# Performance work log

Measured on AMD Instinct MI355X. Metric: run time of the kernel, lower is better.

The kernel has to match this reference:

```python
import jax, jax.numpy as jnp
import numpy as np
from jax import lax


def extract_patches(x, kh, kw, sh, sw):
    # x: [B,H,W,C] -> [B,oh,ow,kh,kw,C], same element order as tf.image.extract_patches
    B, H, W, C = x.shape
    oh = (H - kh) // sh + 1
    ow = (W - kw) // sw + 1
    rows = jnp.arange(oh)[:, None] * sh + jnp.arange(kh)[None, :]  # [oh,kh]
    cols = jnp.arange(ow)[:, None] * sw + jnp.arange(kw)[None, :]  # [ow,kw]
    p = x[:, rows]            # [B,oh,kh,W,C]
    p = p[:, :, :, cols]      # [B,oh,kh,ow,kw,C]
    return jnp.transpose(p, (0, 1, 3, 2, 4, 5))  # [B,oh,ow,kh,kw,C]


def fastgrnn(x, W, U, bg, bu, zeta, nu):
    # FastGRNN: z=sigmoid(Wx+Uh+bg); c=tanh(Wx+Uh+bu); h'=z*h+(sig(zeta)*(1-z)+sig(nu))*c
    # x: [N,T,D] -> final hidden [N,H]
    wx = jnp.einsum('ntd,dh->nth', x, W)  # precompute input projection
    z_gate = jax.nn.sigmoid(zeta)
    n_gate = jax.nn.sigmoid(nu)

    def step(h, wx_t):
        pre = wx_t + h @ U
        z = jax.nn.sigmoid(pre + bg)
        c = jnp.tanh(pre + bu)
        h_new = z * h + (z_gate * (1.0 - z) + n_gate) * c
        return h_new, None

    h0 = jnp.zeros((x.shape[0], W.shape[1]), x.dtype)
    hT, _ = lax.scan(step, h0, jnp.swapaxes(wx, 0, 1))  # scan over T
    return hT


def rnnpool_forward(inputs, W1, U1, bg1, bu1, zeta1, nu1,
                    W2, U2, bg2, bu2, zeta2, nu2, kh, kw, sh, sw):
    B, H, Wd, C = inputs.shape
    oh = (H - kh) // sh + 1
    ow = (Wd - kw) // sw + 1
    patches = extract_patches(inputs, kh, kw, sh, sw)          # [B,oh,ow,kh,kw,C]
    N = B * oh * ow
    p = patches.reshape(N, kh, kw, C)

    u = W1.shape[1]
    # row-wise: rnn1 scans along cols within each row
    x = p.reshape(N * kh, kw, C)
    h = fastgrnn(x, W1, U1, bg1, bu1, zeta1, nu1).reshape(N, kh, u)
    o21 = fastgrnn(h, W2, U2, bg2, bu2, zeta2, nu2)
    o22 = fastgrnn(h[:, ::-1, :], W2, U2, bg2, bu2, zeta2, nu2)

    # col-wise: transpose patch, rnn1 scans along rows within each col
    xc = jnp.transpose(p, (0, 2, 1, 3)).reshape(N * kw, kh, C)
    hc = fastgrnn(xc, W1, U1, bg1, bu1, zeta1, nu1).reshape(N, kw, u)
    o23 = fastgrnn(hc, W2, U2, bg2, bu2, zeta2, nu2)
    o24 = fastgrnn(hc[:, ::-1, :], W2, U2, bg2, bu2, zeta2, nu2)

    out = jnp.concatenate([o21, o22, o23, o24], axis=1)        # [N, 4*hOut]
    return out.reshape(B, oh, ow, -1)


def setup_inputs() -> dict:
    key = jax.random.key(0)
    ks = jax.random.split(key, 9)
    C, u, hout = 16, 8, 16  # in-channels, rnn1 hidden, rnn2 hidden (out_channel//4)
    s = 0.1
    inp = {
        'inputs': jax.random.normal(ks[0], (32, 112, 112, C), jnp.float32),
        'W1': jax.random.normal(ks[1], (C, u), jnp.float32) * s,
        'U1': jax.random.normal(ks[2], (u, u), jnp.float32) * s,
        'bg1': jnp.ones((u,), jnp.float32),
        'bu1': jnp.ones((u,), jnp.float32),
        'zeta1': jnp.float32(100.0),
        'nu1': jnp.float32(-100.0),
        'W2': jax.random.normal(ks[3], (u, hout), jnp.float32) * s,
        'U2': jax.random.normal(ks[4], (hout, hout), jnp.float32) * s,
        'bg2': jnp.ones((hout,), jnp.float32),
        'bu2': jnp.ones((hout,), jnp.float32),
        'zeta2': jnp.float32(100.0),
        'nu2': jnp.float32(-100.0),
        'kh': 8, 'kw': 8, 'sh': 4, 'sw': 4,
    }
    return inp


def reference(inputs, W1, U1, bg1, bu1, zeta1, nu1,
              W2, U2, bg2, bu2, zeta2, nu2, kh, kw, sh, sw):
    return rnnpool_forward(inputs, W1, U1, bg1, bu1, zeta1, nu1,
                           W2, U2, bg2, bu2, zeta2, nu2, kh, kw, sh, sw)
```

## Files before the change

kernel.cpp:

```cpp
#include <hip/hip_runtime.h>

#define PPB 4

typedef float v2f __attribute__((ext_vector_type(2)));

__device__ __forceinline__ float frcp(float x) { return __builtin_amdgcn_rcpf(x); }

__device__ __forceinline__ v2f vfma2(v2f a, v2f b, v2f c) {
#if __has_builtin(__builtin_elementwise_fma)
  return __builtin_elementwise_fma(a, b, c);
#else
  v2f d; d.x = fmaf(a.x, b.x, c.x); d.y = fmaf(a.y, b.y, c.y); return d;
#endif
}
__device__ __forceinline__ v2f vmul2(v2f a, v2f b) { return a * b; }
__device__ __forceinline__ v2f vadd2(v2f a, v2f b) { return a + b; }
__device__ __forceinline__ v2f bc(float x) { v2f p; p.x = x; p.y = x; return p; }

__device__ __forceinline__ v2f gate2(v2f pre, v2f h, v2f bgB, v2f KB, v2f nzgB,
                                     v2f AB, bool first) {
  v2f a = vadd2(pre, bgB);
  v2f s; s.x = __expf(-a.x); s.y = __expf(-a.y);
  v2f one = bc(1.f);
  v2f zd = vadd2(s, one);
  v2f z; z.x = frcp(zd.x); z.y = frcp(zd.y);
  v2f u = vmul2(vmul2(s, s), KB);
  v2f cd = vadd2(u, one);
  v2f cr; cr.x = frcp(cd.x); cr.y = frcp(cd.y);
  v2f cc = vfma2(cr, bc(2.f), bc(-1.f));
  v2f m = vfma2(z, nzgB, AB);
  v2f mc = vmul2(m, cc);
  return first ? mc : vfma2(z, h, mc);
}

__global__ __launch_bounds__(256, 4) void l1_kernel(
    const float* __restrict__ inp, const float* __restrict__ W1,
    const float* __restrict__ U1, const float* __restrict__ bg1,
    const float* __restrict__ bu1, const float* __restrict__ zeta1,
    const float* __restrict__ nu1, float* __restrict__ hrowg,
    float* __restrict__ hcolg) {
  constexpr int ST = 98;

  __shared__ float w1s[128];
  __shared__ float wxs[112 * ST];

  const int tid = threadIdx.x;
  const int bid = blockIdx.x;
  const bool isrow = bid < 448;
  const int v = isrow ? bid : bid - 448;
  const int b = v / 14, wp = v % 14;
  const int base4 = 8 * wp;
  const int span = (wp == 13) ? 8 : 12;

  if (tid < 32) ((float4*)w1s)[tid] = ((const float4*)W1)[tid];
  __syncthreads();

  for (int p = tid; p < 1344; p += 256) {
    int q, s;
    if (isrow) { q = p / 12;  s = p % 12; }
    else       { q = p % 112; s = p / 112; }
    if (s < span) {
      const float* px = isrow
          ? inp + ((size_t)(b * 112 + q) * 112 + base4 + s) * 16
          : inp + ((size_t)(b * 112 + base4 + s) * 112 + q) * 16;
      float4 x0 = ((const float4*)px)[0], x1 = ((const float4*)px)[1],
             x2 = ((const float4*)px)[2], x3 = ((const float4*)px)[3];
      float xr[16] = {x0.x, x0.y, x0.z, x0.w, x1.x, x1.y, x1.z, x1.w,
                      x2.x, x2.y, x2.z, x2.w, x3.x, x3.y, x3.z, x3.w};
      float a0 = 0.f, a1 = 0.f, a2 = 0.f, a3 = 0.f,
            a4 = 0.f, a5 = 0.f, a6 = 0.f, a7 = 0.f;
#pragma unroll
      for (int ci = 0; ci < 16; ++ci) {
        float4 wL = *(const float4*)&w1s[ci * 8];
        float4 wH = *(const float4*)&w1s[ci * 8 + 4];
        a0 = fmaf(xr[ci], wL.x, a0); a1 = fmaf(xr[ci], wL.y, a1);
        a2 = fmaf(xr[ci], wL.z, a2); a3 = fmaf(xr[ci], wL.w, a3);
        a4 = fmaf(xr[ci], wH.x, a4); a5 = fmaf(xr[ci], wH.y, a5);
        a6 = fmaf(xr[ci], wH.z, a6); a7 = fmaf(xr[ci], wH.w, a7);
      }
      float* wd = &wxs[q * ST + s * 8];
      ((float2*)wd)[0] = float2{a0, a1};
      ((float2*)wd)[1] = float2{a2, a3};
      ((float2*)wd)[2] = float2{a4, a5};
      ((float2*)wd)[3] = float2{a6, a7};
    }
  }

  float u1r[8][8];
#pragma unroll
  for (int i = 0; i < 8; i += 2) {
    float4 r0 = ((const float4*)U1)[i * 2 + 0];
    float4 r1 = ((const float4*)U1)[i * 2 + 1];
    float4 r2 = ((const float4*)U1)[i * 2 + 2];
    float4 r3 = ((const float4*)U1)[i * 2 + 3];
    u1r[i][0] = r0.x; u1r[i][1] = r0.y; u1r[i][2] = r0.z; u1r[i][3] = r0.w;
    u1r[i][4] = r1.x; u1r[i][5] = r1.y; u1r[i][6] = r1.z; u1r[i][7] = r1.w;
    u1r[i+1][0] = r2.x; u1r[i+1][1] = r2.y; u1r[i+1][2] = r2.z; u1r[i+1][3] = r2.w;
    u1r[i+1][4] = r3.x; u1r[i+1][5] = r3.y; u1r[i+1][6] = r3.z; u1r[i+1][7] = r3.w;
  }
  float bgv[8], Kc[8];
#pragma unroll
  for (int j = 0; j < 8; ++j) {
    bgv[j] = bg1[j];
    Kc[j] = __expf(2.f * (bg1[j] - bu1[j]));
  }
  const float zg = frcp(1.f + __expf(-zeta1[0]));
  const float ng = frcp(1.f + __expf(-nu1[0]));
  const float A = zg + ng;

  __syncthreads();

  const int nact = (wp == 13) ? 112 : 224;
  if (tid < nact) {
    const int wl = tid / 112, r = tid % 112;
    const int base = r * ST + wl * 32;
    float h[8];
    {
      const float* w0p = &wxs[base];
#pragma unroll
      for (int j = 0; j < 8; ++j) {
        float s = __expf(-(w0p[j] + bgv[j]));
        float z = frcp(1.f + s);
        float u = s * s * Kc[j];
        float c = fmaf(2.f, frcp(1.f + u), -1.f);
        float m = fmaf(-zg, z, A);
        h[j] = m * c;
      }
    }
#pragma unroll
    for (int t = 1; t < 8; ++t) {
      const float* wtp = &wxs[base + t * 8];
      float qa[8];
#pragma unroll
      for (int j = 0; j < 8; ++j) {
        float q = u1r[0][j] * h[0];
        q = fmaf(u1r[1][j], h[1], q);
        q = fmaf(u1r[2][j], h[2], q);
        q = fmaf(u1r[3][j], h[3], q);
        q = fmaf(u1r[4][j], h[4], q);
        q = fmaf(u1r[5][j], h[5], q);
        q = fmaf(u1r[6][j], h[6], q);
        q = fmaf(u1r[7][j], h[7], q);
        qa[j] = q;
      }
#pragma unroll
      for (int j = 0; j < 8; ++j) {
        float pre = wtp[j] + qa[j];
        float s = __expf(-(pre + bgv[j]));
        float z = frcp(1.f + s);
        float u = s * s * Kc[j];
        float c = fmaf(2.f, frcp(1.f + u), -1.f);
        float m = fmaf(-zg, z, A);
        h[j] = fmaf(z, h[j], m * c);
      }
    }
    float* dst = (isrow ? hrowg : hcolg) +
                 ((size_t)(b * 27 + 2 * wp + wl) * 112 + r) * 8;
    ((float4*)dst)[0] = float4{h[0], h[1], h[2], h[3]};
    ((float4*)dst)[1] = float4{h[4], h[5], h[6], h[7]};
  }
}

__global__ __launch_bounds__(256) void l2_kernel(
    const float* __restrict__ hrowg, const float* __restrict__ hcolg,
    const float* __restrict__ W2, const float* __restrict__ U2,
    const float* __restrict__ bg2, const float* __restrict__ bu2,
    const float* __restrict__ zeta2, const float* __restrict__ nu2,
    float* __restrict__ out) {
  constexpr int GST = 18;
  constexpr int WHT = 18;
  __shared__ v2f hbI[PPB][128];
  __shared__ v2f whb[PPB][2 * 8 * WHT];
  __shared__ v2f h2I[PPB][3 * GST + 16];

  const int tid = threadIdx.x, wv = tid >> 6, lane = tid & 63;
  const int w = blockIdx.x * PPB + wv;
  const int n0 = 2 * w, n1 = n0 + 1;

  {
    const int p = lane >> 5, half = (lane >> 4) & 1, idx = lane & 15;
    const int pn = p ? n1 : n0;
    const int pw = pn % 27;
    const int qq = pn / 27;
    const int ph = qq % 27, bb = qq / 27;
    const float* src = half ? &hcolg[(((size_t)(bb * 27 + ph)) * 112 + pw * 4) * 8]
                            : &hrowg[(((size_t)(bb * 27 + pw)) * 112 + ph * 4) * 8];
    float4 val = ((const float4*)src)[idx];
    float* base = (float*)&hbI[wv][half * 64 + idx * 4];
    base[0 + p] = val.x;
    base[2 + p] = val.y;
    base[4 + p] = val.z;
    base[6 + p] = val.w;
  }
  __builtin_amdgcn_wave_barrier();

  const int g = lane >> 4, j = lane & 15;
  v2f w2b[8], u2b[16];
#pragma unroll
  for (int d = 0; d < 8; ++d) w2b[d] = bc(W2[d * 16 + j]);
#pragma unroll
  for (int i = 0; i < 16; ++i) u2b[i] = bc(U2[i * 16 + j]);
  const float bg2v = bg2[j], bu2v = bu2[j];
  const float zg2 = frcp(1.f + __expf(-zeta2[0]));
  const float ng2 = frcp(1.f + __expf(-nu2[0]));
  const v2f bgB = bc(bg2v);
  const v2f KB = bc(__expf(2.f * (bg2v - bu2v)));
  const v2f nzgB = bc(-zg2);
  const v2f AB = bc(zg2 + ng2);

  const int src = g >> 1;

  {
    const v2f* hb = &hbI[wv][src * 64];
    const int t0 = (g & 1) * 4;
#pragma unroll
    for (int i = 0; i < 4; ++i) {
      const int t = t0 + i;
      const v2f* hr = &hb[t * 8];
      v2f p = vmul2(hr[0], w2b[0]);
#pragma unroll
      for (int d = 1; d < 8; ++d) p = vfma2(hr[d], w2b[d], p);
      whb[wv][(src * 8 + t) * WHT + j] = p;
    }
  }
  __builtin_amdgcn_wave_barrier();

  const v2f* whsrc = &whb[wv][src * 8 * WHT];
  v2f* h2q = &h2I[wv][g * GST];

  v2f h2 = bc(0.f);
  {
    const int tt = (g & 1) ? 7 : 0;
    v2f p = whsrc[tt * WHT + j];
    h2 = gate2(p, h2, bgB, KB, nzgB, AB, true);
    h2q[j] = h2;
  }
  __builtin_amdgcn_wave_barrier();
#pragma unroll
  for (int t = 1; t < 8; ++t) {
    const int tt = (g & 1) ? (7 - t) : t;
    v2f p = whsrc[tt * WHT + j];
    const float4* q4 = (const float4*)h2q;
    float4 v0 = q4[0], v1 = q4[1], v2_ = q4[2], v3 = q4[3];
    float4 v4 = q4[4], v5 = q4[5], v6 = q4[6], v7 = q4[7];
    v2f q = vmul2(v2f{v0.x, v0.y}, u2b[0]);
    q = vfma2(v2f{v0.z, v0.w}, u2b[1], q);
    q = vfma2(v2f{v1.x, v1.y}, u2b[2], q);
    q = vfma2(v2f{v1.z, v1.w}, u2b[3], q);
    q = vfma2(v2f{v2_.x, v2_.y}, u2b[4], q);
    q = vfma2(v2f{v2_.z, v2_.w}, u2b[5], q);
    q = vfma2(v2f{v3.x, v3.y}, u2b[6], q);
    q = vfma2(v2f{v3.z, v3.w}, u2b[7], q);
    q = vfma2(v2f{v4.x, v4.y}, u2b[8], q);
    q = vfma2(v2f{v4.z, v4.w}, u2b[9], q);
    q = vfma2(v2f{v5.x, v5.y}, u2b[10], q);
    q = vfma2(v2f{v5.z, v5.w}, u2b[11], q);
    q = vfma2(v2f{v6.x, v6.y}, u2b[12], q);
    q = vfma2(v2f{v6.z, v6.w}, u2b[13], q);
    q = vfma2(v2f{v7.x, v7.y}, u2b[14], q);
    q = vfma2(v2f{v7.z, v7.w}, u2b[15], q);
    v2f pre = vadd2(p, q);
    h2 = gate2(pre, h2, bgB, KB, nzgB, AB, false);
    if (t < 7) {
      h2q[j] = h2;
      __builtin_amdgcn_wave_barrier();
    }
  }

  out[(size_t)n0 * 64 + lane] = h2.x;
  out[(size_t)n1 * 64 + lane] = h2.y;
}

extern "C" void kernel_launch(void* const* d_in, const int* in_sizes, int n_in,
                              void* d_out, int out_size, void* d_ws, size_t ws_size,
                              hipStream_t stream) {
  const float* inp   = (const float*)d_in[0];
  const float* W1    = (const float*)d_in[1];
  const float* U1    = (const float*)d_in[2];
  const float* bg1   = (const float*)d_in[3];
  const float* bu1   = (const float*)d_in[4];
  const float* zeta1 = (const float*)d_in[5];
  const float* nu1   = (const float*)d_in[6];
  const float* W2    = (const float*)d_in[7];
  const float* U2    = (const float*)d_in[8];
  const float* bg2   = (const float*)d_in[9];
  const float* bu2   = (const float*)d_in[10];
  const float* zeta2 = (const float*)d_in[11];
  const float* nu2   = (const float*)d_in[12];
  float* out = (float*)d_out;

  const size_t HSZ = (size_t)32 * 27 * 112 * 8;
  float* hrowg = (float*)d_ws;
  float* hcolg = hrowg + HSZ;

  l1_kernel<<<dim3(896), dim3(256), 0, stream>>>(
      inp, W1, U1, bg1, bu1, zeta1, nu1, hrowg, hcolg);
  l2_kernel<<<dim3(2916), dim3(256), 0, stream>>>(
      hrowg, hcolg, W2, U2, bg2, bu2, zeta2, nu2, out);
}
```

Before: 43.51 us.

## Restructure both RNN kernels: per-thread L2 recurrence and batched L1 projection

The layer-2 kernel switches from a lane-per-hidden-unit layout that communicates through LDS with wave barriers to a layout where each thread carries a full 16-wide hidden state in registers for one patch/direction. It reads weights from uniform global memory and prefetches the next timestep's input. The layer-1 input projection now batches six pixels per thread, reads W1 directly from global instead of LDS, and uses stride 97 in shared memory. These changes are meant to remove LDS round-trips and barriers, at the cost of more registers per thread, 16x more FMAs per thread in the recurrence, and fewer threads overall.

New measurement: 58.52 us. 1.34x slower.

```diff
diff --git a/kernel.cpp b/kernel.cpp
--- a/kernel.cpp
+++ b/kernel.cpp
@@ -1,47 +1,14 @@
 #include <hip/hip_runtime.h>
 
-#define PPB 4
-
-typedef float v2f __attribute__((ext_vector_type(2)));
-
 __device__ __forceinline__ float frcp(float x) { return __builtin_amdgcn_rcpf(x); }
 
-__device__ __forceinline__ v2f vfma2(v2f a, v2f b, v2f c) {
-#if __has_builtin(__builtin_elementwise_fma)
-  return __builtin_elementwise_fma(a, b, c);
-#else
-  v2f d; d.x = fmaf(a.x, b.x, c.x); d.y = fmaf(a.y, b.y, c.y); return d;
-#endif
-}
-__device__ __forceinline__ v2f vmul2(v2f a, v2f b) { return a * b; }
-__device__ __forceinline__ v2f vadd2(v2f a, v2f b) { return a + b; }
-__device__ __forceinline__ v2f bc(float x) { v2f p; p.x = x; p.y = x; return p; }
-
-__device__ __forceinline__ v2f gate2(v2f pre, v2f h, v2f bgB, v2f KB, v2f nzgB,
-                                     v2f AB, bool first) {
-  v2f a = vadd2(pre, bgB);
-  v2f s; s.x = __expf(-a.x); s.y = __expf(-a.y);
-  v2f one = bc(1.f);
-  v2f zd = vadd2(s, one);
-  v2f z; z.x = frcp(zd.x); z.y = frcp(zd.y);
-  v2f u = vmul2(vmul2(s, s), KB);
-  v2f cd = vadd2(u, one);
-  v2f cr; cr.x = frcp(cd.x); cr.y = frcp(cd.y);
-  v2f cc = vfma2(cr, bc(2.f), bc(-1.f));
-  v2f m = vfma2(z, nzgB, AB);
-  v2f mc = vmul2(m, cc);
-  return first ? mc : vfma2(z, h, mc);
-}
-
-__global__ __launch_bounds__(256, 4) void l1_kernel(
+__global__ __launch_bounds__(256) void l1_kernel(
     const float* __restrict__ inp, const float* __restrict__ W1,
     const float* __restrict__ U1, const float* __restrict__ bg1,
     const float* __restrict__ bu1, const float* __restrict__ zeta1,
     const float* __restrict__ nu1, float* __restrict__ hrowg,
     float* __restrict__ hcolg) {
-  constexpr int ST = 98;
-
-  __shared__ float w1s[128];
+  constexpr int ST = 97;
   __shared__ float wxs[112 * ST];
 
   const int tid = threadIdx.x;
@@ -52,52 +19,59 @@
   const int base4 = 8 * wp;
   const int span = (wp == 13) ? 8 : 12;
 
-  if (tid < 32) ((float4*)w1s)[tid] = ((const float4*)W1)[tid];
-  __syncthreads();
-
-  for (int p = tid; p < 1344; p += 256) {
+  int qk[6], sk[6];
+  const float* pk[6];
+  bool actk[6];
+#pragma unroll
+  for (int k = 0; k < 6; ++k) {
+    const int p = tid + 256 * k;
     int q, s;
-    if (isrow) { q = p / 12;  s = p % 12; }
+    if (isrow) { q = p / 12;  s = p - 12 * q; }
     else       { q = p % 112; s = p / 112; }
-    if (s < span) {
-      const float* px = isrow
-          ? inp + ((size_t)(b * 112 + q) * 112 + base4 + s) * 16
-          : inp + ((size_t)(b * 112 + base4 + s) * 112 + q) * 16;
-      float4 x0 = ((const float4*)px)[0], x1 = ((const float4*)px)[1],
-             x2 = ((const float4*)px)[2], x3 = ((const float4*)px)[3];
-      float xr[16] = {x0.x, x0.y, x0.z, x0.w, x1.x, x1.y, x1.z, x1.w,
-                      x2.x, x2.y, x2.z, x2.w, x3.x, x3.y, x3.z, x3.w};
-      float a0 = 0.f, a1 = 0.f, a2 = 0.f, a3 = 0.f,
-            a4 = 0.f, a5 = 0.f, a6 = 0.f, a7 = 0.f;
-#pragma unroll
-      for (int ci = 0; ci < 16; ++ci) {
-        float4 wL = *(const float4*)&w1s[ci * 8];
-        float4 wH = *(const float4*)&w1s[ci * 8 + 4];
-        a0 = fmaf(xr[ci], wL.x, a0); a1 = fmaf(xr[ci], wL.y, a1);
-        a2 = fmaf(xr[ci], wL.z, a2); a3 = fmaf(xr[ci], wL.w, a3);
-        a4 = fmaf(xr[ci], wH.x, a4); a5 = fmaf(xr[ci], wH.y, a5);
-        a6 = fmaf(xr[ci], wH.z, a6); a7 = fmaf(xr[ci], wH.w, a7);
-      }
-      float* wd = &wxs[q * ST + s * 8];
-      ((float2*)wd)[0] = float2{a0, a1};
-      ((float2*)wd)[1] = float2{a2, a3};
-      ((float2*)wd)[2] = float2{a4, a5};
-      ((float2*)wd)[3] = float2{a6, a7};
-    }
-  }
+    qk[k] = q; sk[k] = s;
+    actk[k] = (p < 1344) && (s < span);
+    pk[k] = isrow
+        ? inp + ((size_t)(b * 112 + q) * 112 + base4 + s) * 16
+        : inp + ((size_t)(b * 112 + base4 + s) * 112 + q) * 16;
+  }
+
+  float acc[6][8];
+#pragma unroll
+  for (int k = 0; k < 6; ++k)
+#pragma unroll
+    for (int j = 0; j < 8; ++j) acc[k][j] = 0.f;
+
+#pragma unroll 1
+  for (int half = 0; half < 2; ++half) {
+    const float* w1h = W1 + half * 64;
+#pragma unroll
+    for (int k = 0; k < 6; ++k) {
+      if (actk[k]) {
+        const float4* xp = (const float4*)(pk[k] + half * 8);
+        float4 x0 = xp[0], x1 = xp[1];
+        float xr[8] = {x0.x, x0.y, x0.z, x0.w, x1.x, x1.y, x1.z, x1.w};
+#pragma unroll
+        for (int ci = 0; ci < 8; ++ci)
+#pragma unroll
+          for (int j = 0; j < 8; ++j)
+            acc[k][j] = fmaf(xr[ci], w1h[ci * 8 + j], acc[k][j]);
+      }
+    }
+  }
+
+#pragma unroll
+  for (int k = 0; k < 6; ++k)
+    if (actk[k]) {
+      float* wd = &wxs[qk[k] * ST + sk[k] * 8];
+#pragma unroll
+      for (int j = 0; j < 8; ++j) wd[j] = acc[k][j];
+    }
 
   float u1r[8][8];
 #pragma unroll
-  for (int i = 0; i < 8; i += 2) {
-    float4 r0 = ((const float4*)U1)[i * 2 + 0];
-    float4 r1 = ((const float4*)U1)[i * 2 + 1];
-    float4 r2 = ((const float4*)U1)[i * 2 + 2];
-    float4 r3 = ((const float4*)U1)[i * 2 + 3];
-    u1r[i][0] = r0.x; u1r[i][1] = r0.y; u1r[i][2] = r0.z; u1r[i][3] = r0.w;
-    u1r[i][4] = r1.x; u1r[i][5] = r1.y; u1r[i][6] = r1.z; u1r[i][7] = r1.w;
-    u1r[i+1][0] = r2.x; u1r[i+1][1] = r2.y; u1r[i+1][2] = r2.z; u1r[i+1][3] = r2.w;
-    u1r[i+1][4] = r3.x; u1r[i+1][5] = r3.y; u1r[i+1][6] = r3.z; u1r[i+1][7] = r3.w;
-  }
+  for (int i = 0; i < 8; ++i)
+#pragma unroll
+    for (int j = 0; j < 8; ++j) u1r[i][j] = U1[i * 8 + j];
   float bgv[8], Kc[8];
 #pragma unroll
   for (int j = 0; j < 8; ++j) {
@@ -112,14 +86,13 @@
 
   const int nact = (wp == 13) ? 112 : 224;
   if (tid < nact) {
-    const int wl = tid / 112, r = tid % 112;
+    const int wl = tid / 112, r = tid - 112 * wl;
     const int base = r * ST + wl * 32;
     float h[8];
     {
-      const float* w0p = &wxs[base];
 #pragma unroll
       for (int j = 0; j < 8; ++j) {
-        float s = __expf(-(w0p[j] + bgv[j]));
+        float s = __expf(-(wxs[base + j] + bgv[j]));
         float z = frcp(1.f + s);
         float u = s * s * Kc[j];
         float c = fmaf(2.f, frcp(1.f + u), -1.f);
@@ -129,7 +102,6 @@
     }
 #pragma unroll
     for (int t = 1; t < 8; ++t) {
-      const float* wtp = &wxs[base + t * 8];
       float qa[8];
 #pragma unroll
       for (int j = 0; j < 8; ++j) {
@@ -145,7 +117,7 @@
       }
 #pragma unroll
       for (int j = 0; j < 8; ++j) {
-        float pre = wtp[j] + qa[j];
+        float pre = wxs[base + t * 8 + j] + qa[j];
         float s = __expf(-(pre + bgv[j]));
         float z = frcp(1.f + s);
         float u = s * s * Kc[j];
@@ -161,114 +133,91 @@
   }
 }
 
-__global__ __launch_bounds__(256) void l2_kernel(
+__global__ __launch_bounds__(64) void l2_kernel(
     const float* __restrict__ hrowg, const float* __restrict__ hcolg,
     const float* __restrict__ W2, const float* __restrict__ U2,
     const float* __restrict__ bg2, const float* __restrict__ bu2,
     const float* __restrict__ zeta2, const float* __restrict__ nu2,
     float* __restrict__ out) {
-  constexpr int GST = 18;
-  constexpr int WHT = 18;
-  __shared__ v2f hbI[PPB][128];
-  __shared__ v2f whb[PPB][2 * 8 * WHT];
-  __shared__ v2f h2I[PPB][3 * GST + 16];
-
-  const int tid = threadIdx.x, wv = tid >> 6, lane = tid & 63;
-  const int w = blockIdx.x * PPB + wv;
-  const int n0 = 2 * w, n1 = n0 + 1;
-
+  const int lane = threadIdx.x;
+  const int p = lane >> 2, g = lane & 3;
+  const int n = blockIdx.x * 16 + p;
+  const int pw = n % 27;
+  const int q = n / 27;
+  const int ph = q % 27, b = q / 27;
+  const int rev = g & 1;
+
+  const float* hs = (g < 2)
+      ? &hrowg[((size_t)(b * 27 + pw) * 112 + ph * 4) * 8]
+      : &hcolg[((size_t)(b * 27 + ph) * 112 + pw * 4) * 8];
+
+  float bgv[16], Kc[16];
+#pragma unroll
+  for (int j = 0; j < 16; ++j) {
+    bgv[j] = bg2[j];
+    Kc[j] = __expf(2.f * (bg2[j] - bu2[j]));
+  }
+  const float zg = frcp(1.f + __expf(-zeta2[0]));
+  const float ng = frcp(1.f + __expf(-nu2[0]));
+  const float A = zg + ng;
+
+  float h2[16];
+#pragma unroll
+  for (int j = 0; j < 16; ++j) h2[j] = 0.f;
+
+  float cur[8], nxt[8];
   {
-    const int p = lane >> 5, half = (lane >> 4) & 1, idx = lane & 15;
-    const int pn = p ? n1 : n0;
-    const int pw = pn % 27;
-    const int qq = pn / 27;
-    const int ph = qq % 27, bb = qq / 27;
-    const float* src = half ? &hcolg[(((size_t)(bb * 27 + ph)) * 112 + pw * 4) * 8]
-                            : &hrowg[(((size_t)(bb * 27 + pw)) * 112 + ph * 4) * 8];
-    float4 val = ((const float4*)src)[idx];
-    float* base = (float*)&hbI[wv][half * 64 + idx * 4];
-    base[0 + p] = val.x;
-    base[2 + p] = val.y;
-    base[4 + p] = val.z;
-    base[6 + p] = val.w;
-  }
-  __builtin_amdgcn_wave_barrier();
-
-  const int g = lane >> 4, j = lane & 15;
-  v2f w2b[8], u2b[16];
-#pragma unroll
-  for (int d = 0; d < 8; ++d) w2b[d] = bc(W2[d * 16 + j]);
-#pragma unroll
-  for (int i = 0; i < 16; ++i) u2b[i] = bc(U2[i * 16 + j]);
-  const float bg2v = bg2[j], bu2v = bu2[j];
-  const float zg2 = frcp(1.f + __expf(-zeta2[0]));
-  const float ng2 = frcp(1.f + __expf(-nu2[0]));
-  const v2f bgB = bc(bg2v);
-  const v2f KB = bc(__expf(2.f * (bg2v - bu2v)));
-  const v2f nzgB = bc(-zg2);
-  const v2f AB = bc(zg2 + ng2);
-
-  const int src = g >> 1;
-
-  {
-    const v2f* hb = &hbI[wv][src * 64];
-    const int t0 = (g & 1) * 4;
-#pragma unroll
-    for (int i = 0; i < 4; ++i) {
-      const int t = t0 + i;
-      const v2f* hr = &hb[t * 8];
-      v2f p = vmul2(hr[0], w2b[0]);
-#pragma unroll
-      for (int d = 1; d < 8; ++d) p = vfma2(hr[d], w2b[d], p);
-      whb[wv][(src * 8 + t) * WHT + j] = p;
-    }
-  }
-  __builtin_amdgcn_wave_barrier();
-
-  const v2f* whsrc = &whb[wv][src * 8 * WHT];
-  v2f* h2q = &h2I[wv][g * GST];
-
-  v2f h2 = bc(0.f);
-  {
-    const int tt = (g & 1) ? 7 : 0;
-    v2f p = whsrc[tt * WHT + j];
-    h2 = gate2(p, h2, bgB, KB, nzgB, AB, true);
-    h2q[j] = h2;
-  }
-  __builtin_amdgcn_wave_barrier();
-#pragma unroll
-  for (int t = 1; t < 8; ++t) {
-    const int tt = (g & 1) ? (7 - t) : t;
-    v2f p = whsrc[tt * WHT + j];
-    const float4* q4 = (const float4*)h2q;
-    float4 v0 = q4[0], v1 = q4[1], v2_ = q4[2], v3 = q4[3];
-    float4 v4 = q4[4], v5 = q4[5], v6 = q4[6], v7 = q4[7];
-    v2f q = vmul2(v2f{v0.x, v0.y}, u2b[0]);
-    q = vfma2(v2f{v0.z, v0.w}, u2b[1], q);
-    q = vfma2(v2f{v1.x, v1.y}, u2b[2], q);
-    q = vfma2(v2f{v1.z, v1.w}, u2b[3], q);
-    q = vfma2(v2f{v2_.x, v2_.y}, u2b[4], q);
-    q = vfma2(v2f{v2_.z, v2_.w}, u2b[5], q);
-    q = vfma2(v2f{v3.x, v3.y}, u2b[6], q);
-    q = vfma2(v2f{v3.z, v3.w}, u2b[7], q);
-    q = vfma2(v2f{v4.x, v4.y}, u2b[8], q);
-    q = vfma2(v2f{v4.z, v4.w}, u2b[9], q);
-    q = vfma2(v2f{v5.x, v5.y}, u2b[10], q);
-    q = vfma2(v2f{v5.z, v5.w}, u2b[11], q);
-    q = vfma2(v2f{v6.x, v6.y}, u2b[12], q);
-    q = vfma2(v2f{v6.z, v6.w}, u2b[13], q);
-    q = vfma2(v2f{v7.x, v7.y}, u2b[14], q);
-    q = vfma2(v2f{v7.z, v7.w}, u2b[15], q);
-    v2f pre = vadd2(p, q);
-    h2 = gate2(pre, h2, bgB, KB, nzgB, AB, false);
+    const float4* rp = (const float4*)(hs + (rev ? 7 : 0) * 8);
+    float4 r0 = rp[0], r1 = rp[1];
+    cur[0] = r0.x; cur[1] = r0.y; cur[2] = r0.z; cur[3] = r0.w;
+    cur[4] = r1.x; cur[5] = r1.y; cur[6] = r1.z; cur[7] = r1.w;
+  }
+
+#pragma unroll 1
+  for (int t = 0; t < 8; ++t) {
+    asm volatile("" ::: "memory");
     if (t < 7) {
-      h2q[j] = h2;
-      __builtin_amdgcn_wave_barrier();
-    }
-  }
-
-  out[(size_t)n0 * 64 + lane] = h2.x;
-  out[(size_t)n1 * 64 + lane] = h2.y;
+      const int tt2 = rev ? (6 - t) : (t + 1);
+      const float4* rp = (const float4*)(hs + tt2 * 8);
+      float4 r0 = rp[0], r1 = rp[1];
+      nxt[0] = r0.x; nxt[1] = r0.y; nxt[2] = r0.z; nxt[3] = r0.w;
+      nxt[4] = r1.x; nxt[5] = r1.y; nxt[6] = r1.z; nxt[7] = r1.w;
+    }
+    float pre[16];
+#pragma unroll
+    for (int j = 0; j < 16; ++j) pre[j] = cur[0] * W2[j];
+#pragma unroll
+    for (int d = 1; d < 8; ++d)
+#pragma unroll
+      for (int j = 0; j < 16; ++j)
+        pre[j] = fmaf(cur[d], W2[d * 16 + j], pre[j]);
+    if (t > 0) {
+#pragma unroll
+      for (int i = 0; i < 16; ++i)
+#pragma unroll
+        for (int j = 0; j < 16; ++j)
+          pre[j] = fmaf(h2[i], U2[i * 16 + j], pre[j]);
+    }
+#pragma unroll
+    for (int j = 0; j < 16; ++j) {
+      float s = __expf(-(pre[j] + bgv[j]));
+      float z = frcp(1.f + s);
+      float u = s * s * Kc[j];
+      float c = fmaf(2.f, frcp(1.f + u), -1.f);
+      float m = fmaf(-zg, z, A);
+      h2[j] = fmaf(z, h2[j], m * c);
+    }
+    if (t < 7) {
+#pragma unroll
+      for (int d = 0; d < 8; ++d) cur[d] = nxt[d];
+    }
+  }
+
+  float* op = out + (size_t)n * 64 + g * 16;
+  ((float4*)op)[0] = float4{h2[0], h2[1], h2[2], h2[3]};
+  ((float4*)op)[1] = float4{h2[4], h2[5], h2[6], h2[7]};
+  ((float4*)op)[2] = float4{h2[8], h2[9], h2[10], h2[11]};
+  ((float4*)op)[3] = float4{h2[12], h2[13], h2[14], h2[15]};
 }
 
 extern "C" void kernel_launch(void* const* d_in, const int* in_sizes, int n_in,
@@ -295,6 +244,6 @@
 
   l1_kernel<<<dim3(896), dim3(256), 0, stream>>>(
       inp, W1, U1, bg1, bu1, zeta1, nu1, hrowg, hcolg);
-  l2_kernel<<<dim3(2916), dim3(256), 0, stream>>>(
+  l2_kernel<<<dim3(1458), dim3(64), 0, stream>>>(
       hrowg, hcolg, W2, U2, bg2, bu2, zeta2, nu2, out);
 }
```
